# Kernel tuning notes

Hardware: AMD Instinct MI355X
Metric: run time of the kernel (lower is better)

The kernel has to match this reference:

```python
import jax, jax.numpy as jnp
import numpy as np

N = 50000      # nodes
E = 800000     # edges
D_IN = 128
D_OUT = 128


def setup_inputs() -> dict:
    key = jax.random.key(0)
    k1, k2, k3 = jax.random.split(key, 3)
    x = jax.random.normal(k1, (N, D_IN), dtype=jnp.float32)
    edge_index = jax.random.randint(k2, (2, E), 0, N, dtype=jnp.int32)
    W = jax.random.normal(k3, (D_OUT, D_IN), dtype=jnp.float32) / np.sqrt(D_IN)
    b = jnp.zeros((D_OUT,), dtype=jnp.float32)
    return {"x": x, "edge_index": edge_index, "W": W, "b": b}


def reference(x, edge_index, W, b):
    # PyG GCNConv: add self-loops, symmetric D^{-1/2}(A+I)D^{-1/2} normalization,
    # linear transform, scatter-sum aggregation, then bias.
    n = x.shape[0]
    loop = jnp.arange(n, dtype=edge_index.dtype)
    src = jnp.concatenate([edge_index[0], loop])  # [E+N]
    dst = jnp.concatenate([edge_index[1], loop])  # [E+N]

    # degree over destination nodes (incl. self-loops)
    deg = jax.ops.segment_sum(jnp.ones_like(dst, dtype=x.dtype), dst, num_segments=n)
    dinv = jnp.where(deg > 0, jax.lax.rsqrt(deg), 0.0)
    norm = dinv[src] * dinv[dst]                  # [E+N]

    x_lin = x @ W.T                               # [N, D_OUT]
    msgs = x_lin[src] * norm[:, None]             # gather + scale, [E+N, D_OUT]
    out = jax.ops.segment_sum(msgs, dst, num_segments=n)  # scatter-add
    return out + b
```

## Files before the change

### kernel.cpp

```cpp
#include <hip/hip_runtime.h>
#include <math.h>

#define D_FEAT 128
#define NB1 391
#define EPB 2048
#define NBUCK 782
#define NPB 64
#define SUBCAP 24
#define ELDS 1536
#define CSTRIDE 1664

typedef unsigned int u32;
typedef __bf16 bf16x8 __attribute__((ext_vector_type(8)));
typedef float f32x4 __attribute__((ext_vector_type(4)));

__device__ __forceinline__ unsigned short bf16_rne(float f) {
    unsigned int u = __float_as_uint(f);
    u += 0x7FFFu + ((u >> 16) & 1u);
    return (unsigned short)(u >> 16);
}

__device__ __forceinline__ void split_pack(float a, float b, u32& hi, u32& lo) {
    u32 ua = __float_as_uint(a), ub = __float_as_uint(b);
    u32 ha = ua & 0xffff0000u, hb = ub & 0xffff0000u;
    float ra = a - __uint_as_float(ha);
    float rb = b - __uint_as_float(hb);
    hi = hb | (ua >> 16);
    lo = (__float_as_uint(rb) & 0xffff0000u) | (__float_as_uint(ra) >> 16);
}

__device__ __forceinline__ void split8(const float4& f0, const float4& f1,
                                       uint4& hi, uint4& lo) {
    split_pack(f0.x, f0.y, hi.x, lo.x);
    split_pack(f0.z, f0.w, hi.y, lo.y);
    split_pack(f1.x, f1.y, hi.z, lo.z);
    split_pack(f1.z, f1.w, hi.w, lo.w);
}

__device__ __forceinline__ f32x4 mfma_bf16(uint4 a, uint4 b, f32x4 c) {
    return __builtin_amdgcn_mfma_f32_16x16x32_bf16(
        __builtin_bit_cast(bf16x8, a), __builtin_bit_cast(bf16x8, b), c, 0, 0, 0);
}

__global__ __launch_bounds__(256) void build_gemm_kernel(
    const int* __restrict__ src, const int* __restrict__ dst,
    unsigned int* __restrict__ subbuck, unsigned short* __restrict__ cnt_sub,
    int E, int n,
    const float* __restrict__ A, const float* __restrict__ W,
    unsigned short* __restrict__ y) {
    __shared__ u32 smem[2 * 64 * 68];
    if (blockIdx.x < NB1) {
        int* hist = (int*)smem;
        int t = threadIdx.x;
        int B = blockIdx.x;
        for (int j = t; j < NBUCK; j += 256) hist[j] = 0;
        __syncthreads();
        int base = B * EPB;
        int e8 = base + t * 8;
        int d[8], s[8];
        bool v[8];
        if (e8 + 8 <= E) {
            int4 dd0 = *(const int4*)(dst + e8);
            int4 dd1 = *(const int4*)(dst + e8 + 4);
            int4 ss0 = *(const int4*)(src + e8);
            int4 ss1 = *(const int4*)(src + e8 + 4);
            d[0] = dd0.x; d[1] = dd0.y; d[2] = dd0.z; d[3] = dd0.w;
            d[4] = dd1.x; d[5] = dd1.y; d[6] = dd1.z; d[7] = dd1.w;
            s[0] = ss0.x; s[1] = ss0.y; s[2] = ss0.z; s[3] = ss0.w;
            s[4] = ss1.x; s[5] = ss1.y; s[6] = ss1.z; s[7] = ss1.w;
#pragma unroll
            for (int j = 0; j < 8; ++j) v[j] = true;
        } else {
#pragma unroll
            for (int j = 0; j < 8; ++j) {
                v[j] = e8 + j < E;
                d[j] = v[j] ? dst[e8 + j] : 0;
                s[j] = v[j] ? src[e8 + j] : 0;
            }
        }
        int bk[8], r[8];
        unsigned int pk[8];
#pragma unroll
        for (int j = 0; j < 8; ++j) {
            bk[j] = d[j] >> 6;
            pk[j] = ((unsigned int)(d[j] & 63) << 16) | (unsigned int)s[j];
        }
#pragma unroll
        for (int j = 0; j < 8; ++j)
            r[j] = v[j] ? atomicAdd(&hist[bk[j]], 1) : 0;
        __syncthreads();
        for (int j = t; j < NBUCK; j += 256)
            cnt_sub[(size_t)B * NBUCK + j] = (unsigned short)min(hist[j], SUBCAP);
#pragma unroll
        for (int j = 0; j < 8; ++j)
            if (v[j] && r[j] < SUBCAP)
                subbuck[((size_t)bk[j] * NB1 + B) * SUBCAP + r[j]] = pk[j];
        return;
    }

    int bb = blockIdx.x - NB1;
    int t = threadIdx.x;
    int r0 = (bb >> 1) * 64;
    int c0 = (bb & 1) * 64;
    u32* Whi = smem;
    u32* Wlo = smem + 64 * 68;

    for (int i = t; i < 1024; i += 256) {
        int c = i >> 4;
        int kg = (i & 15) * 8;
        const float* wp = W + (size_t)(c0 + c) * D_FEAT + kg;
        float4 f0 = *(const float4*)wp;
        float4 f1 = *(const float4*)(wp + 4);
        uint4 hi, lo;
        split8(f0, f1, hi, lo);
        int idx = c * 68 + (i & 15) * 4;
        *(uint4*)&Whi[idx] = hi;
        *(uint4*)&Wlo[idx] = lo;
    }
    __syncthreads();

    int lane = t & 63;
    int wv = t >> 6;
    int mrow = r0 + wv * 16 + (lane & 15);
    bool valid = mrow < n;
    int kb = (lane >> 4) * 8;

    uint4 xhiu[4], xlou[4];
    const float* xp = A + (size_t)mrow * D_FEAT + kb;
#pragma unroll
    for (int kt = 0; kt < 4; ++kt) {
        float4 a0, a1;
        if (valid) {
            a0 = *(const float4*)(xp + kt * 32);
            a1 = *(const float4*)(xp + kt * 32 + 4);
        } else {
            a0 = make_float4(0.f, 0.f, 0.f, 0.f);
            a1 = make_float4(0.f, 0.f, 0.f, 0.f);
        }
        split8(a0, a1, xhiu[kt], xlou[kt]);
    }

    f32x4 acc[4];
#pragma unroll
    for (int nt = 0; nt < 4; ++nt) acc[nt] = (f32x4){0.f, 0.f, 0.f, 0.f};

#pragma unroll
    for (int kt = 0; kt < 4; ++kt) {
        uint4 xh = xhiu[kt], xl = xlou[kt];
#pragma unroll
        for (int nt = 0; nt < 4; ++nt) {
            int idx = (nt * 16 + (lane & 15)) * 68 + kt * 16 + (lane >> 4) * 4;
            uint4 wh = *(const uint4*)&Whi[idx];
            uint4 wl = *(const uint4*)&Wlo[idx];
            acc[nt] = mfma_bf16(wh, xh, acc[nt]);
            acc[nt] = mfma_bf16(wl, xh, acc[nt]);
            acc[nt] = mfma_bf16(wh, xl, acc[nt]);
        }
    }

    if (valid) {
        unsigned short* yp = y + (size_t)mrow * D_FEAT + c0 + (lane >> 4) * 4;
#pragma unroll
        for (int nt = 0; nt < 4; ++nt) {
            u32 w0 = (u32)bf16_rne(acc[nt][0]) | ((u32)bf16_rne(acc[nt][1]) << 16);
            u32 w1 = (u32)bf16_rne(acc[nt][2]) | ((u32)bf16_rne(acc[nt][3]) << 16);
            uint2 o;
            o.x = w0;
            o.y = w1;
            *(uint2*)(yp + nt * 16) = o;
        }
    }
}

__global__ __launch_bounds__(256) void bin_kernel(
    const unsigned int* __restrict__ subbuck,
    const unsigned short* __restrict__ cnt_sub,
    unsigned short* __restrict__ csr, uint4* __restrict__ meta,
    float* __restrict__ dinv, int n) {
    __shared__ unsigned int eds[ELDS];
    __shared__ int sarr[512];
    __shared__ int hist[NPB];
    __shared__ int p2[NPB];
    __shared__ int cur[NPB];
    int b = blockIdx.x, t = threadIdx.x;

    int c0 = (t < NB1) ? (int)cnt_sub[(size_t)t * NBUCK + b] : 0;
    int c1 = (t + 256 < NB1) ? (int)cnt_sub[(size_t)(t + 256) * NBUCK + b] : 0;
    sarr[t] = c0;
    sarr[t + 256] = c1;
    if (t < NPB) hist[t] = 0;
    __syncthreads();
    for (int ofs = 1; ofs < 512; ofs <<= 1) {
        int u0 = (t >= ofs) ? sarr[t - ofs] : 0;
        int u1 = (t + 256 >= ofs) ? sarr[t + 256 - ofs] : 0;
        __syncthreads();
        sarr[t] += u0;
        sarr[t + 256] += u1;
        __syncthreads();
    }
    int M = sarr[511];
    if (M > ELDS) M = ELDS;

    {
        int sb = sarr[t] - c0;
        const uint4* sp4 = (const uint4*)(subbuck + ((size_t)b * NB1 + t) * SUBCAP);
        for (int j = 0; j < c0; j += 4) {
            uint4 vq = sp4[j >> 2];
            u32 e4[4] = {vq.x, vq.y, vq.z, vq.w};
#pragma unroll
            for (int k = 0; k < 4; ++k) {
                int idx = j + k;
                if (idx < c0 && sb + idx < ELDS) eds[sb + idx] = e4[k];
            }
        }
    }
    if (t + 256 < NB1) {
        int sb = sarr[t + 256] - c1;
        const uint4* sp4 = (const uint4*)(subbuck + ((size_t)b * NB1 + t + 256) * SUBCAP);
        for (int j = 0; j < c1; j += 4) {
            uint4 vq = sp4[j >> 2];
            u32 e4[4] = {vq.x, vq.y, vq.z, vq.w};
#pragma unroll
            for (int k = 0; k < 4; ++k) {
                int idx = j + k;
                if (idx < c1 && sb + idx < ELDS) eds[sb + idx] = e4[k];
            }
        }
    }
    __syncthreads();

    for (int e = t; e < M; e += 256) atomicAdd(&hist[eds[e] >> 16], 1);
    __syncthreads();

    int node = b * NPB + t;
    bool vn = (t < NPB) && (node < n);
    int deg = (t < NPB) ? hist[t] : 0;
    int tot = vn ? deg + 1 : 0;
    if (t < NPB) sarr[t] = tot;
    __syncthreads();
    for (int ofs = 1; ofs < NPB; ofs <<= 1) {
        int u = (t < NPB && t >= ofs) ? sarr[t - ofs] : 0;
        __syncthreads();
        if (t < NPB) sarr[t] += u;
        __syncthreads();
    }
    if (t < NPB) {
        int pb = sarr[t] - tot;
        p2[t] = pb;
        cur[t] = 0;
        if (vn) {
            int start = b * CSTRIDE + pb;
            float dv = rsqrtf((float)(deg + 1));
            meta[node] = make_uint4((unsigned int)start, (unsigned int)tot,
                                    __float_as_uint(dv), 0u);
            dinv[node] = dv;
            csr[start] = (unsigned short)node;
        }
    }
    __syncthreads();

    for (int e = t; e < M; e += 256) {
        int loc = eds[e] >> 16;
        int sl = atomicAdd(&cur[loc], 1);
        csr[b * CSTRIDE + p2[loc] + 1 + sl] = (unsigned short)(eds[e] & 0xffffu);
    }
}

__global__ __launch_bounds__(256) void agg_kernel(const unsigned short* __restrict__ y,
                                                  const float* __restrict__ dinv,
                                                  const uint4* __restrict__ meta,
                                                  const unsigned short* __restrict__ csr,
                                                  const float* __restrict__ bias,
                                                  float* __restrict__ out, int n) {
    int lane = threadIdx.x & 63;
    int wv = threadIdx.x >> 6;
    int i = blockIdx.x * 4 + wv;
    if (i >= n) return;

    uint4 m = meta[i];
    int start = (int)m.x;
    int tot = (int)m.y;
    float di = __uint_as_float(m.z);
    int tot64 = min(tot, 64);

    int ent = (lane < tot64) ? (int)csr[start + lane] : 0;
    float wgt = (lane < tot64) ? dinv[ent] * di : 0.f;

    int g = lane >> 4;
    int sl = lane & 15;

    float acc[8];
#pragma unroll
    for (int k = 0; k < 8; ++k) acc[k] = 0.f;

    const uint4* yq = (const uint4*)y;
    for (int e = 0; e < tot64; e += 8) {
        int i0 = e + g, i1 = e + 4 + g;
        int s0 = __shfl(ent, min(i0, 63), 64);
        int s1 = __shfl(ent, min(i1, 63), 64);
        float w0 = __shfl(wgt, min(i0, 63), 64);
        float w1 = __shfl(wgt, min(i1, 63), 64);
        bool p0 = i0 < tot64, p1 = i1 < tot64;
        uint4 q0, q1;
        if (p0) q0 = yq[(size_t)s0 * 16 + sl];
        if (p1) q1 = yq[(size_t)s1 * 16 + sl];
        if (p0) {
            acc[0] += __uint_as_float(q0.x << 16) * w0;
            acc[1] += __uint_as_float(q0.x & 0xffff0000u) * w0;
            acc[2] += __uint_as_float(q0.y << 16) * w0;
            acc[3] += __uint_as_float(q0.y & 0xffff0000u) * w0;
            acc[4] += __uint_as_float(q0.z << 16) * w0;
            acc[5] += __uint_as_float(q0.z & 0xffff0000u) * w0;
            acc[6] += __uint_as_float(q0.w << 16) * w0;
            acc[7] += __uint_as_float(q0.w & 0xffff0000u) * w0;
        }
        if (p1) {
            acc[0] += __uint_as_float(q1.x << 16) * w1;
            acc[1] += __uint_as_float(q1.x & 0xffff0000u) * w1;
            acc[2] += __uint_as_float(q1.y << 16) * w1;
            acc[3] += __uint_as_float(q1.y & 0xffff0000u) * w1;
            acc[4] += __uint_as_float(q1.z << 16) * w1;
            acc[5] += __uint_as_float(q1.z & 0xffff0000u) * w1;
            acc[6] += __uint_as_float(q1.w << 16) * w1;
            acc[7] += __uint_as_float(q1.w & 0xffff0000u) * w1;
        }
    }
    for (int e = 64; e < tot; e += 8) {
        int i0 = e + g, i1 = e + 4 + g;
        int s0 = (i0 < tot) ? (int)csr[start + i0] : 0;
        int s1 = (i1 < tot) ? (int)csr[start + i1] : 0;
        float w0 = (i0 < tot) ? dinv[s0] * di : 0.f;
        float w1 = (i1 < tot) ? dinv[s1] * di : 0.f;
        uint4 q0 = yq[(size_t)s0 * 16 + sl];
        uint4 q1 = yq[(size_t)s1 * 16 + sl];
        acc[0] += __uint_as_float(q0.x << 16) * w0;
        acc[1] += __uint_as_float(q0.x & 0xffff0000u) * w0;
        acc[2] += __uint_as_float(q0.y << 16) * w0;
        acc[3] += __uint_as_float(q0.y & 0xffff0000u) * w0;
        acc[4] += __uint_as_float(q0.z << 16) * w0;
        acc[5] += __uint_as_float(q0.z & 0xffff0000u) * w0;
        acc[6] += __uint_as_float(q0.w << 16) * w0;
        acc[7] += __uint_as_float(q0.w & 0xffff0000u) * w0;
        acc[0] += __uint_as_float(q1.x << 16) * w1;
        acc[1] += __uint_as_float(q1.x & 0xffff0000u) * w1;
        acc[2] += __uint_as_float(q1.y << 16) * w1;
        acc[3] += __uint_as_float(q1.y & 0xffff0000u) * w1;
        acc[4] += __uint_as_float(q1.z << 16) * w1;
        acc[5] += __uint_as_float(q1.z & 0xffff0000u) * w1;
        acc[6] += __uint_as_float(q1.w << 16) * w1;
        acc[7] += __uint_as_float(q1.w & 0xffff0000u) * w1;
    }

#pragma unroll
    for (int k = 0; k < 8; ++k) {
        acc[k] += __shfl_xor(acc[k], 16, 64);
        acc[k] += __shfl_xor(acc[k], 32, 64);
    }

    if (lane < 16) {
        const float4* b4 = (const float4*)bias;
        float4 bv0 = b4[sl * 2], bv1 = b4[sl * 2 + 1];
        float4* op = (float4*)(out + (size_t)i * D_FEAT + sl * 8);
        op[0] = make_float4(acc[0] + bv0.x, acc[1] + bv0.y, acc[2] + bv0.z, acc[3] + bv0.w);
        op[1] = make_float4(acc[4] + bv1.x, acc[5] + bv1.y, acc[6] + bv1.z, acc[7] + bv1.w);
    }
}

extern "C" void kernel_launch(void* const* d_in, const int* in_sizes, int n_in,
                              void* d_out, int out_size, void* d_ws, size_t ws_size,
                              hipStream_t stream) {
    const float* x = (const float*)d_in[0];
    const int* ei = (const int*)d_in[1];
    const float* W = (const float*)d_in[2];
    const float* b = (const float*)d_in[3];
    float* out = (float*)d_out;

    int n = in_sizes[0] / D_FEAT;
    int E = in_sizes[1] / 2;
    const int* src = ei;
    const int* dst = ei + E;

    char* ws = (char*)d_ws;
    size_t off = 0;
    auto alloc = [&](size_t bytes) {
        char* p = ws + off;
        off = (off + bytes + 255) & ~(size_t)255;
        return p;
    };
    unsigned int* subbuck = (unsigned int*)alloc((size_t)NBUCK * NB1 * SUBCAP * 4);
    unsigned short* cnt_sub = (unsigned short*)alloc((size_t)NB1 * NBUCK * 2);
    unsigned short* csr = (unsigned short*)alloc((size_t)NBUCK * CSTRIDE * 2);
    uint4* meta = (uint4*)alloc((size_t)n * 16);
    float* dinv = (float*)alloc((size_t)n * 4);
    unsigned short* y = (unsigned short*)alloc((size_t)n * D_FEAT * 2);
    (void)ws_size;

    int gemm_blocks = ((n + 63) / 64) * 2;
    build_gemm_kernel<<<NB1 + gemm_blocks, 256, 0, stream>>>(
        src, dst, subbuck, cnt_sub, E, n, x, W, y);
    bin_kernel<<<NBUCK, 256, 0, stream>>>(subbuck, cnt_sub, csr, meta, dinv, n);
    agg_kernel<<<(n + 3) / 4, 256, 0, stream>>>(y, dinv, meta, csr, b, out, n);
}
```

Baseline: 139.3 us.

## Co-schedule GEMM with fine binning; compute both output halves per block

The dense GEMM moves out of the coarse-binning launch and shares a launch with the fine CSR-building stage, so the GEMM now overlaps the fine binning instead of the coarse pass. Each GEMM block now covers all 128 output columns in two halves, reusing the split X fragments held in registers instead of loading and splitting X twice. The cost is a serialized W reload plus an extra barrier per block, and fewer GEMM blocks to spread across the GPU.

```diff
diff --git a/kernel.cpp b/kernel.cpp
--- a/kernel.cpp
+++ b/kernel.cpp
@@ -42,82 +42,162 @@
         __builtin_bit_cast(bf16x8, a), __builtin_bit_cast(bf16x8, b), c, 0, 0, 0);
 }
 
-__global__ __launch_bounds__(256) void build_gemm_kernel(
+__global__ __launch_bounds__(256) void coarse_bin_kernel(
     const int* __restrict__ src, const int* __restrict__ dst,
     unsigned int* __restrict__ subbuck, unsigned short* __restrict__ cnt_sub,
-    int E, int n,
+    int E) {
+    __shared__ int hist[NBUCK];
+    int t = threadIdx.x;
+    int B = blockIdx.x;
+    for (int j = t; j < NBUCK; j += 256) hist[j] = 0;
+    __syncthreads();
+    int base = B * EPB;
+    int e8 = base + t * 8;
+    int d[8], s[8];
+    bool v[8];
+    if (e8 + 8 <= E) {
+        int4 dd0 = *(const int4*)(dst + e8);
+        int4 dd1 = *(const int4*)(dst + e8 + 4);
+        int4 ss0 = *(const int4*)(src + e8);
+        int4 ss1 = *(const int4*)(src + e8 + 4);
+        d[0] = dd0.x; d[1] = dd0.y; d[2] = dd0.z; d[3] = dd0.w;
+        d[4] = dd1.x; d[5] = dd1.y; d[6] = dd1.z; d[7] = dd1.w;
+        s[0] = ss0.x; s[1] = ss0.y; s[2] = ss0.z; s[3] = ss0.w;
+        s[4] = ss1.x; s[5] = ss1.y; s[6] = ss1.z; s[7] = ss1.w;
+#pragma unroll
+        for (int j = 0; j < 8; ++j) v[j] = true;
+    } else {
+#pragma unroll
+        for (int j = 0; j < 8; ++j) {
+            v[j] = e8 + j < E;
+            d[j] = v[j] ? dst[e8 + j] : 0;
+            s[j] = v[j] ? src[e8 + j] : 0;
+        }
+    }
+    int bk[8], r[8];
+    unsigned int pk[8];
+#pragma unroll
+    for (int j = 0; j < 8; ++j) {
+        bk[j] = d[j] >> 6;
+        pk[j] = ((unsigned int)(d[j] & 63) << 16) | (unsigned int)s[j];
+    }
+#pragma unroll
+    for (int j = 0; j < 8; ++j)
+        r[j] = v[j] ? atomicAdd(&hist[bk[j]], 1) : 0;
+    __syncthreads();
+    for (int j = t; j < NBUCK; j += 256)
+        cnt_sub[(size_t)B * NBUCK + j] = (unsigned short)min(hist[j], SUBCAP);
+#pragma unroll
+    for (int j = 0; j < 8; ++j)
+        if (v[j] && r[j] < SUBCAP)
+            subbuck[((size_t)bk[j] * NB1 + B) * SUBCAP + r[j]] = pk[j];
+}
+
+__global__ __launch_bounds__(256) void fine_gemm_kernel(
+    const unsigned int* __restrict__ subbuck,
+    const unsigned short* __restrict__ cnt_sub,
+    unsigned short* __restrict__ csr, uint4* __restrict__ meta,
+    float* __restrict__ dinv, int n,
     const float* __restrict__ A, const float* __restrict__ W,
     unsigned short* __restrict__ y) {
     __shared__ u32 smem[2 * 64 * 68];
-    if (blockIdx.x < NB1) {
-        int* hist = (int*)smem;
-        int t = threadIdx.x;
-        int B = blockIdx.x;
-        for (int j = t; j < NBUCK; j += 256) hist[j] = 0;
-        __syncthreads();
-        int base = B * EPB;
-        int e8 = base + t * 8;
-        int d[8], s[8];
-        bool v[8];
-        if (e8 + 8 <= E) {
-            int4 dd0 = *(const int4*)(dst + e8);
-            int4 dd1 = *(const int4*)(dst + e8 + 4);
-            int4 ss0 = *(const int4*)(src + e8);
-            int4 ss1 = *(const int4*)(src + e8 + 4);
-            d[0] = dd0.x; d[1] = dd0.y; d[2] = dd0.z; d[3] = dd0.w;
-            d[4] = dd1.x; d[5] = dd1.y; d[6] = dd1.z; d[7] = dd1.w;
-            s[0] = ss0.x; s[1] = ss0.y; s[2] = ss0.z; s[3] = ss0.w;
-            s[4] = ss1.x; s[5] = ss1.y; s[6] = ss1.z; s[7] = ss1.w;
-#pragma unroll
-            for (int j = 0; j < 8; ++j) v[j] = true;
-        } else {
-#pragma unroll
-            for (int j = 0; j < 8; ++j) {
-                v[j] = e8 + j < E;
-                d[j] = v[j] ? dst[e8 + j] : 0;
-                s[j] = v[j] ? src[e8 + j] : 0;
+    int t = threadIdx.x;
+
+    if (blockIdx.x < NBUCK) {
+        unsigned int* eds = smem;
+        int* sarr = (int*)(smem + ELDS);
+        int* hist = (int*)(smem + ELDS + 512);
+        int* p2   = (int*)(smem + ELDS + 576);
+        int* cur  = (int*)(smem + ELDS + 640);
+        int b = blockIdx.x;
+
+        int c0 = (t < NB1) ? (int)cnt_sub[(size_t)t * NBUCK + b] : 0;
+        int c1 = (t + 256 < NB1) ? (int)cnt_sub[(size_t)(t + 256) * NBUCK + b] : 0;
+        sarr[t] = c0;
+        sarr[t + 256] = c1;
+        if (t < NPB) hist[t] = 0;
+        __syncthreads();
+        for (int ofs = 1; ofs < 512; ofs <<= 1) {
+            int u0 = (t >= ofs) ? sarr[t - ofs] : 0;
+            int u1 = (t + 256 >= ofs) ? sarr[t + 256 - ofs] : 0;
+            __syncthreads();
+            sarr[t] += u0;
+            sarr[t + 256] += u1;
+            __syncthreads();
+        }
+        int M = sarr[511];
+        if (M > ELDS) M = ELDS;
+
+        {
+            int sb = sarr[t] - c0;
+            const uint4* sp4 = (const uint4*)(subbuck + ((size_t)b * NB1 + t) * SUBCAP);
+            for (int j = 0; j < c0; j += 4) {
+                uint4 vq = sp4[j >> 2];
+                u32 e4[4] = {vq.x, vq.y, vq.z, vq.w};
+#pragma unroll
+                for (int k = 0; k < 4; ++k) {
+                    int idx = j + k;
+                    if (idx < c0 && sb + idx < ELDS) eds[sb + idx] = e4[k];
+                }
             }
         }
-        int bk[8], r[8];
-        unsigned int pk[8];
-#pragma unroll
-        for (int j = 0; j < 8; ++j) {
-            bk[j] = d[j] >> 6;
-            pk[j] = ((unsigned int)(d[j] & 63) << 16) | (unsigned int)s[j];
-        }
-#pragma unroll
-        for (int j = 0; j < 8; ++j)
-            r[j] = v[j] ? atomicAdd(&hist[bk[j]], 1) : 0;
-        __syncthreads();
-        for (int j = t; j < NBUCK; j += 256)
-            cnt_sub[(size_t)B * NBUCK + j] = (unsigned short)min(hist[j], SUBCAP);
-#pragma unroll
-        for (int j = 0; j < 8; ++j)
-            if (v[j] && r[j] < SUBCAP)
-                subbuck[((size_t)bk[j] * NB1 + B) * SUBCAP + r[j]] = pk[j];
+        if (t + 256 < NB1) {
+            int sb = sarr[t + 256] - c1;
+            const uint4* sp4 = (const uint4*)(subbuck + ((size_t)b * NB1 + t + 256) * SUBCAP);
+            for (int j = 0; j < c1; j += 4) {
+                uint4 vq = sp4[j >> 2];
+                u32 e4[4] = {vq.x, vq.y, vq.z, vq.w};
+#pragma unroll
+                for (int k = 0; k < 4; ++k) {
+                    int idx = j + k;
+                    if (idx < c1 && sb + idx < ELDS) eds[sb + idx] = e4[k];
+                }
+            }
+        }
+        __syncthreads();
+
+        for (int e = t; e < M; e += 256) atomicAdd(&hist[eds[e] >> 16], 1);
+        __syncthreads();
+
+        int node = b * NPB + t;
+        bool vn = (t < NPB) && (node < n);
+        int deg = (t < NPB) ? hist[t] : 0;
+        int tot = vn ? deg + 1 : 0;
+        if (t < NPB) sarr[t] = tot;
+        __syncthreads();
+        for (int ofs = 1; ofs < NPB; ofs <<= 1) {
+            int u = (t < NPB && t >= ofs) ? sarr[t - ofs] : 0;
+            __syncthreads();
+            if (t < NPB) sarr[t] += u;
+            __syncthreads();
+        }
+        if (t < NPB) {
+            int pb = sarr[t] - tot;
+            p2[t] = pb;
+            cur[t] = 0;
+            if (vn) {
+                int start = b * CSTRIDE + pb;
+                float dv = rsqrtf((float)(deg + 1));
+                meta[node] = make_uint4((unsigned int)start, (unsigned int)tot,
+                                        __float_as_uint(dv), 0u);
+                dinv[node] = dv;
+                csr[start] = (unsigned short)node;
+            }
+        }
+        __syncthreads();
+
+        for (int e = t; e < M; e += 256) {
+            int loc = eds[e] >> 16;
+            int sl = atomicAdd(&cur[loc], 1);
+            csr[b * CSTRIDE + p2[loc] + 1 + sl] = (unsigned short)(eds[e] & 0xffffu);
+        }
         return;
     }
 
-    int bb = blockIdx.x - NB1;
-    int t = threadIdx.x;
-    int r0 = (bb >> 1) * 64;
-    int c0 = (bb & 1) * 64;
+    int bb = blockIdx.x - NBUCK;
+    int r0 = bb * 64;
     u32* Whi = smem;
     u32* Wlo = smem + 64 * 68;
-
-    for (int i = t; i < 1024; i += 256) {
-        int c = i >> 4;
-        int kg = (i & 15) * 8;
-        const float* wp = W + (size_t)(c0 + c) * D_FEAT + kg;
-        float4 f0 = *(const float4*)wp;
-        float4 f1 = *(const float4*)(wp + 4);
-        uint4 hi, lo;
-        split8(f0, f1, hi, lo);
-        int idx = c * 68 + (i & 15) * 4;
-        *(uint4*)&Whi[idx] = hi;
-        *(uint4*)&Wlo[idx] = lo;
-    }
-    __syncthreads();
 
     int lane = t & 63;
     int wv = t >> 6;
@@ -140,129 +220,54 @@
         split8(a0, a1, xhiu[kt], xlou[kt]);
     }
 
-    f32x4 acc[4];
-#pragma unroll
-    for (int nt = 0; nt < 4; ++nt) acc[nt] = (f32x4){0.f, 0.f, 0.f, 0.f};
-
-#pragma unroll
-    for (int kt = 0; kt < 4; ++kt) {
-        uint4 xh = xhiu[kt], xl = xlou[kt];
-#pragma unroll
-        for (int nt = 0; nt < 4; ++nt) {
-            int idx = (nt * 16 + (lane & 15)) * 68 + kt * 16 + (lane >> 4) * 4;
-            uint4 wh = *(const uint4*)&Whi[idx];
-            uint4 wl = *(const uint4*)&Wlo[idx];
-            acc[nt] = mfma_bf16(wh, xh, acc[nt]);
-            acc[nt] = mfma_bf16(wl, xh, acc[nt]);
-            acc[nt] = mfma_bf16(wh, xl, acc[nt]);
-        }
-    }
-
-    if (valid) {
-        unsigned short* yp = y + (size_t)mrow * D_FEAT + c0 + (lane >> 4) * 4;
-#pragma unroll
-        for (int nt = 0; nt < 4; ++nt) {
-            u32 w0 = (u32)bf16_rne(acc[nt][0]) | ((u32)bf16_rne(acc[nt][1]) << 16);
-            u32 w1 = (u32)bf16_rne(acc[nt][2]) | ((u32)bf16_rne(acc[nt][3]) << 16);
-            uint2 o;
-            o.x = w0;
-            o.y = w1;
-            *(uint2*)(yp + nt * 16) = o;
-        }
-    }
-}
-
-__global__ __launch_bounds__(256) void bin_kernel(
-    const unsigned int* __restrict__ subbuck,
-    const unsigned short* __restrict__ cnt_sub,
-    unsigned short* __restrict__ csr, uint4* __restrict__ meta,
-    float* __restrict__ dinv, int n) {
-    __shared__ unsigned int eds[ELDS];
-    __shared__ int sarr[512];
-    __shared__ int hist[NPB];
-    __shared__ int p2[NPB];
-    __shared__ int cur[NPB];
-    int b = blockIdx.x, t = threadIdx.x;
-
-    int c0 = (t < NB1) ? (int)cnt_sub[(size_t)t * NBUCK + b] : 0;
-    int c1 = (t + 256 < NB1) ? (int)cnt_sub[(size_t)(t + 256) * NBUCK + b] : 0;
-    sarr[t] = c0;
-    sarr[t + 256] = c1;
-    if (t < NPB) hist[t] = 0;
-    __syncthreads();
-    for (int ofs = 1; ofs < 512; ofs <<= 1) {
-        int u0 = (t >= ofs) ? sarr[t - ofs] : 0;
-        int u1 = (t + 256 >= ofs) ? sarr[t + 256 - ofs] : 0;
-        __syncthreads();
-        sarr[t] += u0;
-        sarr[t + 256] += u1;
-        __syncthreads();
-    }
-    int M = sarr[511];
-    if (M > ELDS) M = ELDS;
-
-    {
-        int sb = sarr[t] - c0;
-        const uint4* sp4 = (const uint4*)(subbuck + ((size_t)b * NB1 + t) * SUBCAP);
-        for (int j = 0; j < c0; j += 4) {
-            uint4 vq = sp4[j >> 2];
-            u32 e4[4] = {vq.x, vq.y, vq.z, vq.w};
-#pragma unroll
-            for (int k = 0; k < 4; ++k) {
-                int idx = j + k;
-                if (idx < c0 && sb + idx < ELDS) eds[sb + idx] = e4[k];
+    for (int half = 0; half < 2; ++half) {
+        int c0 = half * 64;
+        if (half) __syncthreads();
+
+        for (int i = t; i < 1024; i += 256) {
+            int c = i >> 4;
+            int kg = (i & 15) * 8;
+            const float* wp = W + (size_t)(c0 + c) * D_FEAT + kg;
+            float4 f0 = *(const float4*)wp;
+            float4 f1 = *(const float4*)(wp + 4);
+            uint4 hi, lo;
+            split8(f0, f1, hi, lo);
+            int idx = c * 68 + (i & 15) * 4;
+            *(uint4*)&Whi[idx] = hi;
+            *(uint4*)&Wlo[idx] = lo;
+        }
+        __syncthreads();
+
+        f32x4 acc[4];
+#pragma unroll
+        for (int nt = 0; nt < 4; ++nt) acc[nt] = (f32x4){0.f, 0.f, 0.f, 0.f};
+
+#pragma unroll
+        for (int kt = 0; kt < 4; ++kt) {
+            uint4 xh = xhiu[kt], xl = xlou[kt];
+#pragma unroll
+            for (int nt = 0; nt < 4; ++nt) {
+                int idx = (nt * 16 + (lane & 15)) * 68 + kt * 16 + (lane >> 4) * 4;
+                uint4 wh = *(const uint4*)&Whi[idx];
+                uint4 wl = *(const uint4*)&Wlo[idx];
+                acc[nt] = mfma_bf16(wh, xh, acc[nt]);
+                acc[nt] = mfma_bf16(wl, xh, acc[nt]);
+                acc[nt] = mfma_bf16(wh, xl, acc[nt]);
             }
         }
-    }
-    if (t + 256 < NB1) {
-        int sb = sarr[t + 256] - c1;
-        const uint4* sp4 = (const uint4*)(subbuck + ((size_t)b * NB1 + t + 256) * SUBCAP);
-        for (int j = 0; j < c1; j += 4) {
-            uint4 vq = sp4[j >> 2];
-            u32 e4[4] = {vq.x, vq.y, vq.z, vq.w};
-#pragma unroll
-            for (int k = 0; k < 4; ++k) {
-                int idx = j + k;
-                if (idx < c1 && sb + idx < ELDS) eds[sb + idx] = e4[k];
+
+        if (valid) {
+            unsigned short* yp = y + (size_t)mrow * D_FEAT + c0 + (lane >> 4) * 4;
+#pragma unroll
+            for (int nt = 0; nt < 4; ++nt) {
+                u32 w0 = (u32)bf16_rne(acc[nt][0]) | ((u32)bf16_rne(acc[nt][1]) << 16);
+                u32 w1 = (u32)bf16_rne(acc[nt][2]) | ((u32)bf16_rne(acc[nt][3]) << 16);
+                uint2 o;
+                o.x = w0;
+                o.y = w1;
+                *(uint2*)(yp + nt * 16) = o;
             }
         }
-    }
-    __syncthreads();
-
-    for (int e = t; e < M; e += 256) atomicAdd(&hist[eds[e] >> 16], 1);
-    __syncthreads();
-
-    int node = b * NPB + t;
-    bool vn = (t < NPB) && (node < n);
-    int deg = (t < NPB) ? hist[t] : 0;
-    int tot = vn ? deg + 1 : 0;
-    if (t < NPB) sarr[t] = tot;
-    __syncthreads();
-    for (int ofs = 1; ofs < NPB; ofs <<= 1) {
-        int u = (t < NPB && t >= ofs) ? sarr[t - ofs] : 0;
-        __syncthreads();
-        if (t < NPB) sarr[t] += u;
-        __syncthreads();
-    }
-    if (t < NPB) {
-        int pb = sarr[t] - tot;
-        p2[t] = pb;
-        cur[t] = 0;
-        if (vn) {
-            int start = b * CSTRIDE + pb;
-            float dv = rsqrtf((float)(deg + 1));
-            meta[node] = make_uint4((unsigned int)start, (unsigned int)tot,
-                                    __float_as_uint(dv), 0u);
-            dinv[node] = dv;
-            csr[start] = (unsigned short)node;
-        }
-    }
-    __syncthreads();
-
-    for (int e = t; e < M; e += 256) {
-        int loc = eds[e] >> 16;
-        int sl = atomicAdd(&cur[loc], 1);
-        csr[b * CSTRIDE + p2[loc] + 1 + sl] = (unsigned short)(eds[e] & 0xffffu);
     }
 }
 
@@ -395,9 +400,9 @@
     unsigned short* y = (unsigned short*)alloc((size_t)n * D_FEAT * 2);
     (void)ws_size;
 
-    int gemm_blocks = ((n + 63) / 64) * 2;
-    build_gemm_kernel<<<NB1 + gemm_blocks, 256, 0, stream>>>(
-        src, dst, subbuck, cnt_sub, E, n, x, W, y);
-    bin_kernel<<<NBUCK, 256, 0, stream>>>(subbuck, cnt_sub, csr, meta, dinv, n);
+    int gemm_blocks = (n + 63) / 64;
+    coarse_bin_kernel<<<NB1, 256, 0, stream>>>(src, dst, subbuck, cnt_sub, E);
+    fine_gemm_kernel<<<NBUCK + gemm_blocks, 256, 0, stream>>>(
+        subbuck, cnt_sub, csr, meta, dinv, n, x, W, y);
     agg_kernel<<<(n + 3) / 4, 256, 0, stream>>>(y, dinv, meta, csr, b, out, n);
 }
```

After: 140.4 us. About the same (+0.8%).
